# Kernel tuning notes

Measured on AMD Instinct MI355X. Metric: run time of the kernel, lower is better.

Reference implementation:

```python
import jax, jax.numpy as jnp
import numpy as np

T = 8
TAU = 2.0       # spikingjelly LIFNode default tau
VTH = 1.0       # default v_threshold
ALPHA = 2.0     # surrogate.ATan alpha
EPS = 1e-5      # BatchNorm eps


@jax.custom_vjp
def spike_fn(x):
    # Heaviside with ATan surrogate gradient
    return (x >= 0.0).astype(x.dtype)

def _spike_fwd(x):
    return (x >= 0.0).astype(x.dtype), x

def _spike_bwd(x, g):
    sg = (ALPHA / 2.0) / (1.0 + (jnp.pi / 2.0 * ALPHA * x) ** 2)
    return (g * sg,)

spike_fn.defvjp(_spike_fwd, _spike_bwd)


def lif(x_seq):
    """Multi-step LIF over leading time axis. decay_input=True, hard reset to 0, detach_reset."""
    def step(v, x):
        v = v + (x - v) / TAU            # charge
        s = spike_fn(v - VTH)            # fire (surrogate grad)
        v = v * (1.0 - jax.lax.stop_gradient(s))  # detached hard reset to v_reset=0
        return v, s
    _, s_seq = jax.lax.scan(step, jnp.zeros_like(x_seq[0]), x_seq)
    return s_seq


def conv2d(x, w, b, stride):
    y = jax.lax.conv_general_dilated(x, w, (stride, stride), 'VALID',
                                     dimension_numbers=('NCHW', 'OIHW', 'NCHW'))
    return y + b[None, :, None, None]


def batchnorm(x, g, b):
    # training-mode BN over merged (T*B, H, W) axes, matching step_mode='m' BatchNorm2d
    m = x.mean((0, 2, 3), keepdims=True)
    v = x.var((0, 2, 3), keepdims=True)
    return g[None, :, None, None] * (x - m) * jax.lax.rsqrt(v + EPS) + b[None, :, None, None]


def setup_inputs() -> dict:
    key = jax.random.key(0)
    ks = jax.random.split(key, 12)
    def w_init(k, shape):
        fan_in = int(np.prod(shape[1:]))
        return jax.random.normal(k, shape, dtype=jnp.float32) / np.sqrt(fan_in)
    x = jax.random.normal(ks[0], (128, 4, 84, 84), dtype=jnp.float32)
    return {
        'x': x,
        'conv1_w': w_init(ks[1], (32, 4, 8, 8)),  'conv1_b': jnp.zeros((32,), jnp.float32),
        'bn1_g': jnp.ones((32,), jnp.float32),    'bn1_b': jnp.zeros((32,), jnp.float32),
        'conv2_w': w_init(ks[2], (64, 32, 4, 4)), 'conv2_b': jnp.zeros((64,), jnp.float32),
        'bn2_g': jnp.ones((64,), jnp.float32),    'bn2_b': jnp.zeros((64,), jnp.float32),
        'conv3_w': w_init(ks[3], (64, 64, 3, 3)), 'conv3_b': jnp.zeros((64,), jnp.float32),
        'bn3_g': jnp.ones((64,), jnp.float32),    'bn3_b': jnp.zeros((64,), jnp.float32),
        'fc1_w': w_init(ks[4], (512, 3136)),      'fc1_b': jnp.zeros((512,), jnp.float32),
        'fco_w': w_init(ks[5], (2, 512)),         'fco_b': jnp.zeros((2,), jnp.float32),
    }


def reference(x, conv1_w, conv1_b, bn1_g, bn1_b, conv2_w, conv2_b, bn2_g, bn2_b,
              conv3_w, conv3_b, bn3_g, bn3_b, fc1_w, fc1_b, fco_w, fco_b):
    B = x.shape[0]
    # replicate input over T timesteps; fold T into batch for conv/BN (step_mode='m')
    xs = jnp.broadcast_to(x, (T,) + x.shape).reshape((T * B,) + x.shape[1:])

    h = batchnorm(conv2d(xs, conv1_w, conv1_b, 4), bn1_g, bn1_b)   # [TB,32,20,20]
    s = lif(h.reshape((T, B) + h.shape[1:]))
    h = s.reshape((T * B,) + s.shape[2:])

    h = batchnorm(conv2d(h, conv2_w, conv2_b, 2), bn2_g, bn2_b)    # [TB,64,9,9]
    s = lif(h.reshape((T, B) + h.shape[1:]))
    h = s.reshape((T * B,) + s.shape[2:])

    h = batchnorm(conv2d(h, conv3_w, conv3_b, 1), bn3_g, bn3_b)    # [TB,64,7,7]
    s = lif(h.reshape((T, B) + h.shape[1:]))                        # [T,B,64,7,7]

    feat = s.reshape(T, B, -1)                                      # [T,B,3136]
    hid = lif(jnp.einsum('tbi,oi->tbo', feat, fc1_w) + fc1_b)       # [T,B,512]
    out_seq = jnp.einsum('tbo,ko->tbk', hid, fco_w) + fco_b         # [T,B,2]
    return out_seq.mean(0)                                          # [B,2]
```

## Files before the change

kernel.cpp:

```cpp
#include <hip/hip_runtime.h>
#include <cstdint>
#include <cstddef>

#define TT 8

#define E2_ELEMS (128*64*81)
#define E3_ELEMS (128*64*49)

typedef __attribute__((ext_vector_type(8))) short short8;
typedef __attribute__((ext_vector_type(4))) short short4v;
typedef __attribute__((ext_vector_type(4))) float f32x4;

#define BAR_LDS() do { asm volatile("s_waitcnt lgkmcnt(0)" ::: "memory"); \
                       __builtin_amdgcn_s_barrier(); } while (0)

__device__ __forceinline__ void gld_lds16(const void* g, void* l) {
  __builtin_amdgcn_global_load_lds((const __attribute__((address_space(1))) void*)g,
                                   (__attribute__((address_space(3))) void*)l, 16, 0, 0);
}

__device__ __forceinline__ void split3(float v, ushort& h, ushort& m, ushort& l) {
  union { __bf16 b; ushort u; } H, M, L;
  H.b = (__bf16)v; float r1 = v - (float)H.b;
  M.b = (__bf16)r1; float r2 = r1 - (float)M.b;
  L.b = (__bf16)r2;
  h = H.u; m = M.u; l = L.u;
}

__device__ __forceinline__ short8 ld8(const ushort* p) {
  union { short4v h[2]; short8 v; } U;
  U.h[0] = *(const short4v*)(p);
  U.h[1] = *(const short4v*)(p + 4);
  return U.v;
}

__device__ __forceinline__ void bn_wave_stats(const float* __restrict__ p0,
                                              const float* __restrict__ p1,
                                              int ln, float n,
                                              float* __restrict__ stm,
                                              float* __restrict__ str, int cl) {
  float a0 = p0[ln]       + p0[ln + 256];
  float a2 = p0[ln + 128] + p0[ln + 384];
  float a1 = p0[ln + 64]  + p0[ln + 320];
  float a3 = p0[ln + 192] + p0[ln + 448];
  float s  = (a0 + a2) + (a1 + a3);
  float q0 = p1[ln]       + p1[ln + 256];
  float q2 = p1[ln + 128] + p1[ln + 384];
  float q1 = p1[ln + 64]  + p1[ln + 320];
  float q3 = p1[ln + 192] + p1[ln + 448];
  float sq = (q0 + q2) + (q1 + q3);
  #pragma unroll
  for (int mask = 32; mask >= 1; mask >>= 1) {
    s  += __shfl_xor(s,  mask);
    sq += __shfl_xor(sq, mask);
  }
  if (ln == 0) {
    float m = s / n;
    float var = sq / n - m * m;
    stm[cl] = m;
    str[cl] = rsqrtf(var + 1e-5f);
  }
}

__global__ __launch_bounds__(256) void prep_all(const float* __restrict__ w1,
                                                const float* __restrict__ w2,
                                                const float* __restrict__ w3,
                                                const float* __restrict__ wfc,
                                                __bf16* __restrict__ w1f,
                                                __bf16* __restrict__ w2f,
                                                __bf16* __restrict__ w3f,
                                                __bf16* __restrict__ wff) {
  __shared__ float tile[12544];
  int bxx = blockIdx.x;
  int tid = threadIdx.x;

  if (bxx >= 912) {
    int bx2 = bxx - 912;
    int oc0 = (bx2 >> 3) * 32;
    int ci0 = (bx2 & 7) * 8;
    for (int f = tid; f < 12544; f += 256) {
      int oc_l = f / 392, r = f - oc_l * 392;
      tile[f] = wfc[(size_t)(oc0 + oc_l) * 3136 + ci0 * 49 + r];
    }
    __syncthreads();
    int squad = (ci0 & 31) >> 3;
    int sadd  = ci0 >> 5;
    for (int g = tid; g < 1568; g += 256) {
      int pos = g >> 5, oc_l = g & 31;
      union { __bf16 h[8]; uint4 u; } T0, T1, T2;
      #pragma unroll
      for (int j = 0; j < 8; j++) {
        float wv = tile[oc_l * 392 + j * 49 + pos];
        float hf = (float)(__bf16)wv;
        float r1 = wv - hf;
        float mf = (float)(__bf16)r1;
        float r2 = r1 - mf;
        T0.h[j] = (__bf16)wv; T1.h[j] = (__bf16)r1; T2.h[j] = (__bf16)r2;
      }
      int s = pos * 2 + sadd;
      size_t b0 = (((size_t)s * 4 + squad) * 512 + oc0 + oc_l) * 8;
      *(uint4*)(wff + b0)           = T0.u;
      *(uint4*)(wff + b0 + 1605632) = T1.u;
      *(uint4*)(wff + b0 + 3211264) = T2.u;
    }
    return;
  }

  int i = bxx * 256 + tid;
  if (i < 98304) {
    int v = i;
    int j    = v & 7;
    int oc   = (v >> 3) & 63;
    int quad = (v >> 9) & 3;
    int ksg  = (v >> 11) & 15;
    int term = v >> 15;
    int k = ksg * 32 + quad * 8 + j;
    int ci = k >> 4, kpos = k & 15;
    float w = w2[oc * 512 + ci * 16 + kpos];
    float hf = (float)(__bf16)w;
    float r1 = w - hf;
    float mf = (float)(__bf16)r1;
    float r2 = r1 - mf;
    w2f[v] = (term == 0) ? (__bf16)w : (term == 1) ? (__bf16)r1 : (__bf16)r2;
  } else if (i < 208896) {
    int v = i - 98304;
    int j    = v & 7;
    int oc   = (v >> 3) & 63;
    int quad = (v >> 9) & 3;
    int tk   = v >> 11;
    int term = tk / 18, kstep = tk % 18;
    int k = kstep * 32 + quad * 8 + j;
    int pos = k >> 6, ci = k & 63;
    float w = w3[oc * 576 + ci * 9 + pos];
    float hf = (float)(__bf16)w;
    float r1 = w - hf;
    float mf = (float)(__bf16)r1;
    float r2 = r1 - mf;
    w3f[v] = (term == 0) ? (__bf16)w : (term == 1) ? (__bf16)r1 : (__bf16)r2;
  } else {
    int v = i - 208896;
    int j    = v & 7;
    int oc   = (v >> 3) & 31;
    int quad = (v >> 8) & 3;
    int ks   = (v >> 10) & 7;
    int term = v >> 13;
    int k = ks * 32 + quad * 8 + j;
    float w = w1[oc * 256 + k];
    float hf = (float)(__bf16)w;
    float r1 = w - hf;
    float mf = (float)(__bf16)r1;
    float r2 = r1 - mf;
    w1f[v] = (term == 0) ? (__bf16)w : (term == 1) ? (__bf16)r1 : (__bf16)r2;
  }
}

__global__ __launch_bounds__(128) void k_conv1m(const float* __restrict__ x,
                                                const __bf16* __restrict__ w1f,
                                                const float* __restrict__ bias,
                                                float* __restrict__ out,
                                                float* __restrict__ pout) {
  __shared__ ushort xs[24192];
  int tid = threadIdx.x;
  int bx = blockIdx.x;
  int img = bx >> 2, q = bx & 3;
  const float* xb = x + (size_t)img * 28224 + q * 1680;
  for (int f = tid; f < 2016; f += 128) {
    int ci = f / 504, rr = f - ci * 504;
    int row = rr / 21, c4 = rr - row * 21;
    float4 v4 = *(const float4*)(xb + ci * 7056 + row * 84 + c4 * 4);
    union { ushort s[4]; uint2 u; } H, M, L;
    float vv[4] = {v4.x, v4.y, v4.z, v4.w};
    #pragma unroll
    for (int j = 0; j < 4; j++) split3(vv[j], H.s[j], M.s[j], L.s[j]);
    int eo = ci * 2016 + row * 84 + c4 * 4;
    *(uint2*)(xs + eo)         = H.u;
    *(uint2*)(xs + 8064 + eo)  = M.u;
    *(uint2*)(xs + 16128 + eo) = L.u;
  }
  __syncthreads();
  int nh = tid >> 6, lane = tid & 63;
  int l15 = lane & 15, quad = lane >> 4;
  int aoff[7];
  #pragma unroll
  for (int mt = 0; mt < 7; mt++) {
    int px = mt * 16 + l15; if (px > 99) px = 99;
    int oy = px / 20, ox = px - oy * 20;
    aoff[mt] = oy * 336 + ox * 4;
  }
  f32x4 acc[7];
  #pragma unroll
  for (int mt = 0; mt < 7; mt++) acc[mt] = (f32x4){0.f, 0.f, 0.f, 0.f};
  const __bf16* wpb = w1f + quad * 256 + (nh * 16 + l15) * 8;
  for (int ks = 0; ks < 8; ks++) {
    const __bf16* wp = wpb + ks * 1024;
    short8 bh = *(const short8*)(wp);
    short8 bm = *(const short8*)(wp + 8192);
    short8 bl = *(const short8*)(wp + 16384);
    int pair = ks * 4 + quad;
    int e0 = (pair >> 3) * 2016 + (pair & 7) * 84;
    short8 ah[7], am[7], al[7];
    #pragma unroll
    for (int mt = 0; mt < 7; mt++) {
      int e = e0 + aoff[mt];
      ah[mt] = ld8(xs + e);
      am[mt] = ld8(xs + 8064 + e);
      al[mt] = ld8(xs + 16128 + e);
    }
    #pragma unroll
    for (int mt = 0; mt < 7; mt++)
      acc[mt] = __builtin_amdgcn_mfma_f32_16x16x32_bf16(ah[mt], bh, acc[mt], 0, 0, 0);
    #pragma unroll
    for (int mt = 0; mt < 7; mt++)
      acc[mt] = __builtin_amdgcn_mfma_f32_16x16x32_bf16(ah[mt], bm, acc[mt], 0, 0, 0);
    #pragma unroll
    for (int mt = 0; mt < 7; mt++)
      acc[mt] = __builtin_amdgcn_mfma_f32_16x16x32_bf16(am[mt], bh, acc[mt], 0, 0, 0);
    #pragma unroll
    for (int mt = 0; mt < 7; mt++)
      acc[mt] = __builtin_amdgcn_mfma_f32_16x16x32_bf16(am[mt], bm, acc[mt], 0, 0, 0);
    #pragma unroll
    for (int mt = 0; mt < 7; mt++)
      acc[mt] = __builtin_amdgcn_mfma_f32_16x16x32_bf16(ah[mt], bl, acc[mt], 0, 0, 0);
    #pragma unroll
    for (int mt = 0; mt < 7; mt++)
      acc[mt] = __builtin_amdgcn_mfma_f32_16x16x32_bf16(al[mt], bh, acc[mt], 0, 0, 0);
    #pragma unroll
    for (int mt = 0; mt < 7; mt++)
      acc[mt] = __builtin_amdgcn_mfma_f32_16x16x32_bf16(am[mt], bl, acc[mt], 0, 0, 0);
    #pragma unroll
    for (int mt = 0; mt < 7; mt++)
      acc[mt] = __builtin_amdgcn_mfma_f32_16x16x32_bf16(al[mt], bm, acc[mt], 0, 0, 0);
  }
  int oc = nh * 16 + l15;
  float bv = bias[oc];
  float sl = 0.f, sl2 = 0.f;
  float* op = out + (size_t)img * 12800 + oc * 400 + q * 100;
  #pragma unroll
  for (int mt = 0; mt < 7; mt++) {
    int pxb = mt * 16 + quad * 4;
    #pragma unroll
    for (int r = 0; r < 4; r++) {
      int px = pxb + r;
      if (px < 100) {
        float v = acc[mt][r] + bv;
        op[px] = v;
        sl += v; sl2 += v * v;
      }
    }
  }
  __syncthreads();
  float* sred = (float*)xs;
  sred[oc * 4 + quad] = sl;
  sred[128 + oc * 4 + quad] = sl2;
  __syncthreads();
  if (tid < 32) {
    float s  = sred[tid*4] + sred[tid*4+1] + sred[tid*4+2] + sred[tid*4+3];
    float s2 = sred[128+tid*4] + sred[128+tid*4+1] + sred[128+tid*4+2] + sred[128+tid*4+3];
    pout[tid * 512 + bx] = s;
    pout[16384 + tid * 512 + bx] = s2;
  }
}

__global__ void k_bnfinal2(const float* __restrict__ pin, int sqoff, float n,
                           float* __restrict__ meanArr, float* __restrict__ rstdArr) {
  __shared__ float l0[256], l1[256];
  int c = blockIdx.x, tid = threadIdx.x;
  l0[tid] = pin[c * 512 + tid] + pin[c * 512 + tid + 256];
  l1[tid] = pin[sqoff + c * 512 + tid] + pin[sqoff + c * 512 + tid + 256];
  __syncthreads();
  for (int k = 128; k > 0; k >>= 1) {
    if (tid < k) { l0[tid] += l0[tid + k]; l1[tid] += l1[tid + k]; }
    __syncthreads();
  }
  if (tid == 0) {
    float m = l0[0] / n;
    float var = l1[0] / n - m * m;
    meanArr[c] = m;
    rstdArr[c] = rsqrtf(var + 1e-5f);
  }
}

__global__ void k_lif1b(const float* __restrict__ h, const float* __restrict__ mean,
                        const float* __restrict__ rstd, const float* __restrict__ g,
                        const float* __restrict__ bb, uint32_t* __restrict__ sout) {
  int idx = blockIdx.x * 256 + threadIdx.x;
  int ic = idx / 20;
  int ci = ic & 31;
  const float* hp = h + (size_t)idx * 20;
  float gm = g[ci], mm = mean[ci], rs = rstd[ci], bc = bb[ci];
  float xv[20];
  #pragma unroll
  for (int j4 = 0; j4 < 5; j4++) {
    float4 hv = ((const float4*)hp)[j4];
    xv[j4 * 4 + 0] = gm * (hv.x - mm) * rs + bc;
    xv[j4 * 4 + 1] = gm * (hv.y - mm) * rs + bc;
    xv[j4 * 4 + 2] = gm * (hv.z - mm) * rs + bc;
    xv[j4 * 4 + 3] = gm * (hv.w - mm) * rs + bc;
  }
  float v[20];
  #pragma unroll
  for (int j = 0; j < 20; j++) v[j] = 0.f;
  #pragma unroll
  for (int t = 0; t < TT; t++) {
    uint32_t w = 0;
    #pragma unroll
    for (int j = 0; j < 20; j++) {
      v[j] = v[j] + (xv[j] - v[j]) * 0.5f;
      uint32_t s = (v[j] >= 1.0f);
      w |= s << j;
      if (s) v[j] = 0.f;
    }
    sout[t * 81920 + idx] = w;
  }
}

__global__ __launch_bounds__(256) void k_conv2m(const uint32_t* __restrict__ s1b,
                                                const __bf16* __restrict__ wf,
                                                const float* __restrict__ bias,
                                                float* __restrict__ out,
                                                float* __restrict__ pout) {
  __shared__ uint32_t sp[1280];
  __shared__ uint4 wl4[3072];
  __bf16* wl = (__bf16*)wl4;
  int tid = threadIdx.x;
  int img0 = blockIdx.x * 2;
  {
    const uint32_t* src = s1b + (size_t)img0 * 640;
    for (int i = tid; i < 1280; i += 256) sp[i] = src[i];
  }
  int wave = tid >> 6, lane = tid & 63;
  int img_local = wave >> 1;
  int nh = wave & 1;
  int l15 = lane & 15, quad = lane >> 4;
  int ci_off = quad >> 1;
  int kyp = (quad & 1) * 2;
  int spb[6], sh[6];
  #pragma unroll
  for (int mt = 0; mt < 6; mt++) {
    int px = mt * 16 + l15;
    if (px > 80) px = 80;
    int oy = px / 9, ox = px - oy * 9;
    sh[mt]  = ox * 2;
    spb[mt] = img_local * 640 + ci_off * 20 + oy * 2 + kyp;
  }
  f32x4 acc[6][2];
  #pragma unroll
  for (int mt = 0; mt < 6; mt++)
    #pragma unroll
    for (int nt = 0; nt < 2; nt++) acc[mt][nt] = (f32x4){0.f, 0.f, 0.f, 0.f};

  for (int kc = 0; kc < 4; kc++) {
    __syncthreads();
    for (int o = tid * 8; o < 24576; o += 2048) {
      int tk = o >> 11;
      int term = tk >> 2, ksl = tk & 3;
      const __bf16* src = wf + (((term * 16 + kc * 4 + ksl)) << 11) + (o & 2047);
      gld_lds16(src, wl + o);
    }
    __syncthreads();
    #pragma unroll
    for (int ks = 0; ks < 4; ks++) {
      int ksg = kc * 4 + ks;
      short8 a[6];
      #pragma unroll
      for (int mt = 0; mt < 6; mt++) {
        uint32_t w0 = sp[spb[mt] + ksg * 40];
        uint32_t w1 = sp[spb[mt] + ksg * 40 + 1];
        uint32_t n0 = (w0 >> sh[mt]) & 15u;
        uint32_t n1 = (w1 >> sh[mt]) & 15u;
        union { uint32_t u[4]; short8 v; } A;
        A.u[0] = ((n0 & 1u) ? 0x3F80u : 0u) | ((n0 & 2u) ? 0x3F800000u : 0u);
        A.u[1] = ((n0 & 4u) ? 0x3F80u : 0u) | ((n0 & 8u) ? 0x3F800000u : 0u);
        A.u[2] = ((n1 & 1u) ? 0x3F80u : 0u) | ((n1 & 2u) ? 0x3F800000u : 0u);
        A.u[3] = ((n1 & 4u) ? 0x3F80u : 0u) | ((n1 & 8u) ? 0x3F800000u : 0u);
        a[mt] = A.v;
      }
      #pragma unroll
      for (int term = 0; term < 3; term++) {
        int fb = ((term * 4 + ks) << 11) + (quad << 9);
        #pragma unroll
        for (int nt = 0; nt < 2; nt++) {
          short8 b = *(const short8*)(wl + fb + ((((nh << 1) | nt) << 4) + l15) * 8);
          #pragma unroll
          for (int mt = 0; mt < 6; mt++)
            acc[mt][nt] = __builtin_amdgcn_mfma_f32_16x16x32_bf16(a[mt], b, acc[mt][nt], 0, 0, 0);
        }
      }
    }
  }
  float sl[2], sl2[2];
  #pragma unroll
  for (int nt = 0; nt < 2; nt++) {
    sl[nt] = 0.f; sl2[nt] = 0.f;
    int oc = nh * 32 + nt * 16 + l15;
    float bv = bias[oc];
    float* op = out + ((size_t)(img0 + img_local) * 64 + oc) * 81;
    #pragma unroll
    for (int mt = 0; mt < 6; mt++) {
      int pxr = mt * 16 + quad * 4;
      #pragma unroll
      for (int r = 0; r < 4; r++) {
        int px = pxr + r;
        if (px < 81) {
          float v = acc[mt][nt][r] + bv;
          op[px] = v;
          sl[nt] += v; sl2[nt] += v * v;
        }
      }
    }
  }
  __syncthreads();
  float* sred = (float*)wl4;
  #pragma unroll
  for (int nt = 0; nt < 2; nt++) {
    int oc = nh * 32 + nt * 16 + l15;
    int idx = oc * 8 + img_local * 4 + quad;
    sred[idx] = sl[nt];
    sred[512 + idx] = sl2[nt];
  }
  __syncthreads();
  if (tid < 64) {
    float s = 0.f, s2 = 0.f;
    #pragma unroll
    for (int k = 0; k < 8; k++) { s += sred[tid * 8 + k]; s2 += sred[512 + tid * 8 + k]; }
    pout[tid * 512 + blockIdx.x] = s;
    pout[32768 + tid * 512 + blockIdx.x] = s2;
  }
}

__global__ __launch_bounds__(256) void k_lifb2T(const float* __restrict__ h,
                                                const float* __restrict__ bnp,
                                                const float* __restrict__ g,
                                                const float* __restrict__ bb,
                                                uint32_t* __restrict__ s2T) {
  __shared__ uint32_t sb[288];
  __shared__ float stm[32], str[32];
  int b = blockIdx.x, half = blockIdx.y;
  int tid = threadIdx.x;
  int wavei = tid >> 6, ln = tid & 63;
  for (int cl = wavei; cl < 32; cl += 4) {
    int c = half * 32 + cl;
    bn_wave_stats(bnp + c * 512, bnp + 32768 + c * 512, ln, 82944.f, stm, str, cl);
  }
  __syncthreads();
  int c1 = half * 32 + tid / 9, py1 = tid % 9;
  bool has2 = tid < 32;
  int r2 = tid + 256;
  int c2i = half * 32 + r2 / 9, py2 = r2 % 9;
  float gm1 = g[c1], mm1 = stm[tid / 9], rs1 = str[tid / 9], bc1 = bb[c1];
  float gm2 = 0.f, mm2 = 0.f, rs2 = 0.f, bc2 = 0.f;
  if (has2) { gm2 = g[c2i]; mm2 = stm[r2 / 9]; rs2 = str[r2 / 9]; bc2 = bb[c2i]; }
  float v1[9], v2[9];
  #pragma unroll
  for (int j = 0; j < 9; j++) { v1[j] = 0.f; v2[j] = 0.f; }
  size_t base1 = ((size_t)b * 64 + c1) * 81 + py1 * 9;
  size_t base2 = has2 ? ((size_t)b * 64 + c2i) * 81 + py2 * 9 : base1;
  float c1v[9], c2v[9];
  {
    const float* hp = h;
    #pragma unroll
    for (int j = 0; j < 9; j++) c1v[j] = hp[base1 + j];
    if (has2) {
      #pragma unroll
      for (int j = 0; j < 9; j++) c2v[j] = hp[base2 + j];
    }
  }
  #pragma unroll 1
  for (int t = 0; t < TT; t++) {
    float n1v[9], n2v[9];
    if (t < TT - 1) {
      const float* hp = h + (size_t)(t + 1) * E2_ELEMS;
      #pragma unroll
      for (int j = 0; j < 9; j++) n1v[j] = hp[base1 + j];
      if (has2) {
        #pragma unroll
        for (int j = 0; j < 9; j++) n2v[j] = hp[base2 + j];
      }
    }
    uint32_t w = 0;
    #pragma unroll
    for (int j = 0; j < 9; j++) {
      float xv = gm1 * (c1v[j] - mm1) * rs1 + bc1;
      v1[j] = v1[j] + (xv - v1[j]) * 0.5f;
      uint32_t s = (v1[j] >= 1.0f);
      w |= s << j;
      if (s) v1[j] = 0.f;
    }
    sb[tid] = w;
    if (has2) {
      uint32_t w2 = 0;
      #pragma unroll
      for (int j = 0; j < 9; j++) {
        float xv = gm2 * (c2v[j] - mm2) * rs2 + bc2;
        v2[j] = v2[j] + (xv - v2[j]) * 0.5f;
        uint32_t s = (v2[j] >= 1.0f);
        w2 |= s << j;
        if (s) v2[j] = 0.f;
      }
      sb[r2] = w2;
    }
    BAR_LDS();
    if (tid < 81) {
      int r = tid / 9, cpix = tid - r * 9;
      uint32_t wo = 0;
      #pragma unroll
      for (int ci = 0; ci < 32; ci++)
        wo |= ((sb[ci * 9 + r] >> cpix) & 1u) << ci;
      s2T[(size_t)(t * 128 + b) * 162 + tid * 2 + half] = wo;
    }
    BAR_LDS();
    if (t < TT - 1) {
      #pragma unroll
      for (int j = 0; j < 9; j++) c1v[j] = n1v[j];
      if (has2) {
        #pragma unroll
        for (int j = 0; j < 9; j++) c2v[j] = n2v[j];
      }
    }
  }
}

__global__ __launch_bounds__(256) void k_conv3m(const uint32_t* __restrict__ s2T,
                                                const __bf16* __restrict__ wf,
                                                const float* __restrict__ bias,
                                                float* __restrict__ out,
                                                float* __restrict__ pout) {
  __shared__ uint32_t sp[324];
  __shared__ uint4 wl4[4608];
  __bf16* wl = (__bf16*)wl4;
  int tid = threadIdx.x;
  int img0 = blockIdx.x * 2;
  {
    const uint32_t* src = s2T + (size_t)img0 * 162;
    for (int i = tid; i < 324; i += 256) sp[i] = src[i];
  }
  int wave = tid >> 6, lane = tid & 63;
  int img_local = wave >> 1, nh = wave & 1;
  int l15 = lane & 15, quad = lane >> 4;
  int qsh = quad * 8;
  int base[4];
  #pragma unroll
  for (int mt = 0; mt < 4; mt++) {
    int px = mt * 16 + l15;
    if (px > 48) px = 48;
    int oy = px / 7, ox = px - oy * 7;
    base[mt] = img_local * 162 + (oy * 9 + ox) * 2;
  }
  f32x4 acc[4][2];
  #pragma unroll
  for (int mt = 0; mt < 4; mt++)
    #pragma unroll
    for (int nt = 0; nt < 2; nt++) acc[mt][nt] = (f32x4){0.f, 0.f, 0.f, 0.f};

  #pragma unroll
  for (int kc = 0; kc < 3; kc++) {
    __syncthreads();
    #pragma unroll
    for (int it = 0; it < 18; it++) {
      const __bf16* s = wf + (((it / 6) * 18 + kc * 6 + (it % 6)) << 11) + tid * 8;
      gld_lds16(s, wl + (it << 11) + tid * 8);
    }
    __syncthreads();
    #pragma unroll
    for (int ksl = 0; ksl < 6; ksl++) {
      int kstep = kc * 6 + ksl;
      int pos = kstep >> 1, cihalf = kstep & 1;
      int ky = pos / 3, kx = pos % 3;
      short8 a[4];
      #pragma unroll
      for (int mt = 0; mt < 4; mt++) {
        uint32_t word = sp[base[mt] + (ky * 9 + kx) * 2 + cihalf];
        uint32_t byt = (word >> qsh) & 255u;
        union { uint32_t u[4]; short8 v; } A;
        A.u[0] = ((byt & 1u)  ? 0x3F80u : 0u) | ((byt & 2u)   ? 0x3F800000u : 0u);
        A.u[1] = ((byt & 4u)  ? 0x3F80u : 0u) | ((byt & 8u)   ? 0x3F800000u : 0u);
        A.u[2] = ((byt & 16u) ? 0x3F80u : 0u) | ((byt & 32u)  ? 0x3F800000u : 0u);
        A.u[3] = ((byt & 64u) ? 0x3F80u : 0u) | ((byt & 128u) ? 0x3F800000u : 0u);
        a[mt] = A.v;
      }
      #pragma unroll
      for (int term = 0; term < 3; term++) {
        int fb = ((term * 6 + ksl) << 11) + (quad << 9);
        #pragma unroll
        for (int nt = 0; nt < 2; nt++) {
          short8 b = *(const short8*)(wl + fb + ((((nh << 1) | nt) << 4) + l15) * 8);
          #pragma unroll
          for (int mt = 0; mt < 4; mt++)
            acc[mt][nt] = __builtin_amdgcn_mfma_f32_16x16x32_bf16(a[mt], b, acc[mt][nt], 0, 0, 0);
        }
      }
    }
  }
  float sl[2], sl2[2];
  #pragma unroll
  for (int nt = 0; nt < 2; nt++) {
    sl[nt] = 0.f; sl2[nt] = 0.f;
    int oc = nh * 32 + nt * 16 + l15;
    float bv = bias[oc];
    float* op = out + ((size_t)(img0 + img_local) * 64 + oc) * 49;
    #pragma unroll
    for (int mt = 0; mt < 4; mt++) {
      int pxr = mt * 16 + quad * 4;
      #pragma unroll
      for (int r = 0; r < 4; r++) {
        int px = pxr + r;
        if (px < 49) {
          float v = acc[mt][nt][r] + bv;
          op[px] = v;
          sl[nt] += v; sl2[nt] += v * v;
        }
      }
    }
  }
  __syncthreads();
  float* sred = (float*)wl4;
  #pragma unroll
  for (int nt = 0; nt < 2; nt++) {
    int oc = nh * 32 + nt * 16 + l15;
    int idx = oc * 8 + img_local * 4 + quad;
    sred[idx] = sl[nt];
    sred[512 + idx] = sl2[nt];
  }
  __syncthreads();
  if (tid < 64) {
    float s = 0.f, s2 = 0.f;
    #pragma unroll
    for (int k = 0; k < 8; k++) { s += sred[tid * 8 + k]; s2 += sred[512 + tid * 8 + k]; }
    pout[tid * 512 + blockIdx.x] = s;
    pout[32768 + tid * 512 + blockIdx.x] = s2;
  }
}

__global__ __launch_bounds__(256) void k_lifb3T(const float* __restrict__ h,
                                                const float* __restrict__ bnp,
                                                const float* __restrict__ g,
                                                const float* __restrict__ bb,
                                                uint32_t* __restrict__ s3T) {
  __shared__ uint32_t sb[224];
  __shared__ float stm[32], str[32];
  int b = blockIdx.x, half = blockIdx.y;
  int tid = threadIdx.x;
  int wavei = tid >> 6, ln = tid & 63;
  for (int cl = wavei; cl < 32; cl += 4) {
    int c = half * 32 + cl;
    bn_wave_stats(bnp + c * 512, bnp + 32768 + c * 512, ln, 50176.f, stm, str, cl);
  }
  __syncthreads();
  bool active = tid < 224;
  int row = active ? tid : 0;
  int c = half * 32 + row / 7, py = row % 7;
  float gm = g[c], mm = stm[row / 7], rs = str[row / 7], bc = bb[c];
  float v[7];
  #pragma unroll
  for (int j = 0; j < 7; j++) v[j] = 0.f;
  size_t base = ((size_t)b * 64 + c) * 49 + py * 7;
  float cv[7];
  if (active) {
    #pragma unroll
    for (int j = 0; j < 7; j++) cv[j] = h[base + j];
  }
  #pragma unroll 1
  for (int t = 0; t < TT; t++) {
    float nv[7];
    if (active && t < TT - 1) {
      const float* hp = h + (size_t)(t + 1) * E3_ELEMS;
      #pragma unroll
      for (int j = 0; j < 7; j++) nv[j] = hp[base + j];
    }
    if (active) {
      uint32_t w = 0;
      #pragma unroll
      for (int j = 0; j < 7; j++) {
        float xv = gm * (cv[j] - mm) * rs + bc;
        v[j] = v[j] + (xv - v[j]) * 0.5f;
        uint32_t s = (v[j] >= 1.0f);
        w |= s << j;
        if (s) v[j] = 0.f;
      }
      sb[tid] = w;
    }
    BAR_LDS();
    if (tid < 49) {
      int py2 = tid / 7, px = tid - py2 * 7;
      uint32_t wo = 0;
      #pragma unroll
      for (int ci = 0; ci < 32; ci++)
        wo |= ((sb[ci * 7 + py2] >> px) & 1u) << ci;
      s3T[(size_t)(t * 128 + b) * 98 + tid * 2 + half] = wo;
    }
    BAR_LDS();
    if (active && t < TT - 1) {
      #pragma unroll
      for (int j = 0; j < 7; j++) cv[j] = nv[j];
    }
  }
}

__global__ __launch_bounds__(256) void k_fc1m(const uint32_t* __restrict__ s3T,
                                              const __bf16* __restrict__ wf,
                                              float* __restrict__ f1) {
  __shared__ uint32_t aS[6272];
  int tid = threadIdx.x;
  int row0 = blockIdx.x * 64;
  int oc0  = blockIdx.y * 16;
  {
    const uint32_t* src = s3T + (size_t)row0 * 98;
    for (int i = tid; i < 6272; i += 256) aS[i] = src[i];
  }
  __syncthreads();
  int wave = tid >> 6, lane = tid & 63;
  int l15 = lane & 15, quad = lane >> 4;
  int qsh = quad * 8;
  f32x4 acc[4];
  #pragma unroll
  for (int mt = 0; mt < 4; mt++) acc[mt] = (f32x4){0.f, 0.f, 0.f, 0.f};
  int nIter = (wave < 2) ? 25 : 24;
  #pragma unroll 2
  for (int i = 0; i < nIter; i++) {
    int ks = i * 4 + wave;
    short8 a[4];
    #pragma unroll
    for (int mt = 0; mt < 4; mt++) {
      uint32_t word = aS[(mt * 16 + l15) * 98 + ks];
      uint32_t byt = (word >> qsh) & 255u;
      union { uint32_t u[4]; short8 v; } A;
      A.u[0] = ((byt & 1u)  ? 0x3F80u : 0u) | ((byt & 2u)   ? 0x3F800000u : 0u);
      A.u[1] = ((byt & 4u)  ? 0x3F80u : 0u) | ((byt & 8u)   ? 0x3F800000u : 0u);
      A.u[2] = ((byt & 16u) ? 0x3F80u : 0u) | ((byt & 32u)  ? 0x3F800000u : 0u);
      A.u[3] = ((byt & 64u) ? 0x3F80u : 0u) | ((byt & 128u) ? 0x3F800000u : 0u);
      a[mt] = A.v;
    }
    #pragma unroll
    for (int term = 0; term < 3; term++) {
      size_t fb = ((size_t)((term * 98 + ks) * 4 + quad) * 512 + oc0 + l15) * 8;
      short8 b = *(const short8*)(wf + fb);
      #pragma unroll
      for (int mt = 0; mt < 4; mt++)
        acc[mt] = __builtin_amdgcn_mfma_f32_16x16x32_bf16(a[mt], b, acc[mt], 0, 0, 0);
    }
  }
  __syncthreads();
  float* red = (float*)aS;
  #pragma unroll
  for (int mt = 0; mt < 4; mt++)
    #pragma unroll
    for (int r = 0; r < 4; r++)
      red[(wave * 64 + lane) * 17 + mt * 4 + r] = acc[mt][r];
  __syncthreads();
  #pragma unroll
  for (int k = 0; k < 4; k++) {
    int oi = tid + k * 256;
    int row_l = oi >> 4, oc_l = oi & 15;
    int mt = row_l >> 4, rem = row_l & 15;
    int q2 = rem >> 2, r = rem & 3;
    int ln = q2 * 16 + oc_l;
    float s = red[(0 * 64 + ln) * 17 + mt * 4 + r];
    s += red[(1 * 64 + ln) * 17 + mt * 4 + r];
    s += red[(2 * 64 + ln) * 17 + mt * 4 + r];
    s += red[(3 * 64 + ln) * 17 + mt * 4 + r];
    f1[(size_t)(row0 + row_l) * 512 + oc0 + oc_l] = s;
  }
}

__global__ __launch_bounds__(256) void k_fc1fco(const float* __restrict__ f1,
                                                const float* __restrict__ bias,
                                                const float* __restrict__ w,
                                                const float* __restrict__ fcob,
                                                float* __restrict__ out) {
  int b = blockIdx.x, tid = threadIdx.x;
  int o0 = tid, o1 = tid + 256;
  float bv0 = bias[o0], bv1 = bias[o1];
  float w00 = w[o0], w10 = w[512 + o0];
  float w01 = w[o1], w11 = w[512 + o1];
  float x0[TT], x1[TT];
  #pragma unroll
  for (int t = 0; t < TT; t++) {
    x0[t] = f1[(size_t)(t * 128 + b) * 512 + o0];
    x1[t] = f1[(size_t)(t * 128 + b) * 512 + o1];
  }
  float v0 = 0.f, v1 = 0.f;
  float a0 = 0.f, a1 = 0.f;
  #pragma unroll
  for (int t = 0; t < TT; t++) {
    float s0 = x0[t] + bv0;
    v0 = v0 + (s0 - v0) * 0.5f;
    bool sp0 = (v0 >= 1.0f);
    if (sp0) v0 = 0.f;
    float s1 = x1[t] + bv1;
    v1 = v1 + (s1 - v1) * 0.5f;
    bool sp1 = (v1 >= 1.0f);
    if (sp1) v1 = 0.f;
    if (sp0) { a0 += w00; a1 += w10; }
    if (sp1) { a0 += w01; a1 += w11; }
  }
  __shared__ float l0[256], l1[256];
  l0[tid] = a0; l1[tid] = a1; __syncthreads();
  for (int k = 128; k > 0; k >>= 1) {
    if (tid < k) { l0[tid] += l0[tid + k]; l1[tid] += l1[tid + k]; }
    __syncthreads();
  }
  if (tid == 0) {
    out[b * 2 + 0] = l0[0] * 0.125f + fcob[0];
    out[b * 2 + 1] = l1[0] * 0.125f + fcob[1];
  }
}

extern "C" void kernel_launch(void* const* d_in, const int* in_sizes, int n_in,
                              void* d_out, int out_size, void* d_ws, size_t ws_size,
                              hipStream_t stream) {
  const float* x    = (const float*)d_in[0];
  const float* c1w  = (const float*)d_in[1];
  const float* c1b  = (const float*)d_in[2];
  const float* bn1g = (const float*)d_in[3];
  const float* bn1b = (const float*)d_in[4];
  const float* c2w  = (const float*)d_in[5];
  const float* c2b  = (const float*)d_in[6];
  const float* bn2g = (const float*)d_in[7];
  const float* bn2b = (const float*)d_in[8];
  const float* c3w  = (const float*)d_in[9];
  const float* c3b  = (const float*)d_in[10];
  const float* bn3g = (const float*)d_in[11];
  const float* bn3b = (const float*)d_in[12];
  const float* fc1w = (const float*)d_in[13];
  const float* fc1b = (const float*)d_in[14];
  const float* fcow = (const float*)d_in[15];
  const float* fcob = (const float*)d_in[16];
  float* out = (float*)d_out;

  char* ws = (char*)d_ws;
  float*    h1     = (float*)(ws + 0);
  uint32_t* s1bits = (uint32_t*)(ws + 6553600);
  float*    h2     = (float*)(ws + 19660800);
  float*    h3     = (float*)(ws + 46202880);
  __bf16*   w2f    = (__bf16*)(ws + 60882944);
  __bf16*   w3f    = (__bf16*)(ws + 61079552);
  uint32_t* s2T    = (uint32_t*)(ws + 61300736);
  __bf16*   w1f    = (__bf16*)(ws + 62390272);
  float*    st     = (float*)(ws + 64880640);
  __bf16*   wff    = (__bf16*)(ws + 67108864);
  float*    f1sum  = (float*)(ws + 76742656);
  uint32_t* s3T    = (uint32_t*)(ws + 85131264);
  float*    bnpA   = (float*)(ws + 85532672);
  float*    bnpB   = (float*)(ws + 85794816);

  prep_all   <<<1040, 256, 0, stream>>>(c1w, c2w, c3w, fc1w, w1f, w2f, w3f, wff);

  k_conv1m   <<<512, 128, 0, stream>>>(x, w1f, c1b, h1, bnpA);
  k_bnfinal2 <<<32, 256, 0, stream>>>(bnpA, 16384, 51200.f, st, st + 32);
  k_lif1b    <<<320, 256, 0, stream>>>(h1, st, st + 32, bn1g, bn1b, s1bits);

  k_conv2m   <<<512, 256, 0, stream>>>(s1bits, w2f, c2b, h2, bnpB);
  k_lifb2T   <<<dim3(128, 2), 256, 0, stream>>>(h2, bnpB, bn2g, bn2b, s2T);

  k_conv3m   <<<512, 256, 0, stream>>>(s2T, w3f, c3b, h3, bnpB);
  k_lifb3T   <<<dim3(128, 2), 256, 0, stream>>>(h3, bnpB, bn3g, bn3b, s3T);

  k_fc1m     <<<dim3(16, 32), 256, 0, stream>>>(s3T, wff, f1sum);
  k_fc1fco   <<<128, 256, 0, stream>>>(f1sum, fc1b, fcow, fcob, out);
}
```

Baseline: 238.4 us.

## Double-buffer conv2/conv3 weight staging to overlap loads with MFMA

Replaces the large chunked weight staging in the conv2 and conv3 kernels with per-k-step double buffering. The next k-step's weights are fetched into one LDS buffer while MFMAs run on the other, with a vmcnt+barrier between steps. This is meant to hide global-to-LDS load latency and shrink LDS use from 48-72KB to 24KB per block, which may raise occupancy. The cost is more barriers, one per k-step instead of one per chunk.

Result: slower. 243.3 us (+2.1%).

```diff
diff --git a/kernel.cpp b/kernel.cpp
--- a/kernel.cpp
+++ b/kernel.cpp
@@ -13,6 +13,9 @@
 
 #define BAR_LDS() do { asm volatile("s_waitcnt lgkmcnt(0)" ::: "memory"); \
                        __builtin_amdgcn_s_barrier(); } while (0)
+
+#define BAR_VM() do { asm volatile("s_waitcnt vmcnt(0) lgkmcnt(0)" ::: "memory"); \
+                      __builtin_amdgcn_s_barrier(); } while (0)
 
 __device__ __forceinline__ void gld_lds16(const void* g, void* l) {
   __builtin_amdgcn_global_load_lds((const __attribute__((address_space(1))) void*)g,
@@ -320,8 +323,10 @@
                                                 float* __restrict__ out,
                                                 float* __restrict__ pout) {
   __shared__ uint32_t sp[1280];
-  __shared__ uint4 wl4[3072];
-  __bf16* wl = (__bf16*)wl4;
+  __shared__ uint4 bufA4[768];
+  __shared__ uint4 bufB4[768];
+  __bf16* bufA = (__bf16*)bufA4;
+  __bf16* bufB = (__bf16*)bufB4;
   int tid = threadIdx.x;
   int img0 = blockIdx.x * 2;
   {
@@ -349,45 +354,53 @@
     #pragma unroll
     for (int nt = 0; nt < 2; nt++) acc[mt][nt] = (f32x4){0.f, 0.f, 0.f, 0.f};
 
-  for (int kc = 0; kc < 4; kc++) {
-    __syncthreads();
-    for (int o = tid * 8; o < 24576; o += 2048) {
-      int tk = o >> 11;
-      int term = tk >> 2, ksl = tk & 3;
-      const __bf16* src = wf + (((term * 16 + kc * 4 + ksl)) << 11) + (o & 2047);
-      gld_lds16(src, wl + o);
-    }
-    __syncthreads();
-    #pragma unroll
-    for (int ks = 0; ks < 4; ks++) {
-      int ksg = kc * 4 + ks;
-      short8 a[6];
-      #pragma unroll
-      for (int mt = 0; mt < 6; mt++) {
-        uint32_t w0 = sp[spb[mt] + ksg * 40];
-        uint32_t w1 = sp[spb[mt] + ksg * 40 + 1];
-        uint32_t n0 = (w0 >> sh[mt]) & 15u;
-        uint32_t n1 = (w1 >> sh[mt]) & 15u;
-        union { uint32_t u[4]; short8 v; } A;
-        A.u[0] = ((n0 & 1u) ? 0x3F80u : 0u) | ((n0 & 2u) ? 0x3F800000u : 0u);
-        A.u[1] = ((n0 & 4u) ? 0x3F80u : 0u) | ((n0 & 8u) ? 0x3F800000u : 0u);
-        A.u[2] = ((n1 & 1u) ? 0x3F80u : 0u) | ((n1 & 2u) ? 0x3F800000u : 0u);
-        A.u[3] = ((n1 & 4u) ? 0x3F80u : 0u) | ((n1 & 8u) ? 0x3F800000u : 0u);
-        a[mt] = A.v;
-      }
-      #pragma unroll
-      for (int term = 0; term < 3; term++) {
-        int fb = ((term * 4 + ks) << 11) + (quad << 9);
+  auto STAGE = [&](int ksg, __bf16* dst) {
+    #pragma unroll
+    for (int term = 0; term < 3; term++)
+      gld_lds16(wf + (((term * 16 + ksg)) << 11) + tid * 8, dst + term * 2048 + tid * 8);
+  };
+  auto COMPUTE = [&](int ksg, const __bf16* wl) {
+    short8 a[6];
+    #pragma unroll
+    for (int mt = 0; mt < 6; mt++) {
+      uint32_t w0 = sp[spb[mt] + ksg * 40];
+      uint32_t w1 = sp[spb[mt] + ksg * 40 + 1];
+      uint32_t n0 = (w0 >> sh[mt]) & 15u;
+      uint32_t n1 = (w1 >> sh[mt]) & 15u;
+      union { uint32_t u[4]; short8 v; } A;
+      A.u[0] = ((n0 & 1u) ? 0x3F80u : 0u) | ((n0 & 2u) ? 0x3F800000u : 0u);
+      A.u[1] = ((n0 & 4u) ? 0x3F80u : 0u) | ((n0 & 8u) ? 0x3F800000u : 0u);
+      A.u[2] = ((n1 & 1u) ? 0x3F80u : 0u) | ((n1 & 2u) ? 0x3F800000u : 0u);
+      A.u[3] = ((n1 & 4u) ? 0x3F80u : 0u) | ((n1 & 8u) ? 0x3F800000u : 0u);
+      a[mt] = A.v;
+    }
+    #pragma unroll
+    for (int term = 0; term < 3; term++) {
+      int fb = (term << 11) + (quad << 9);
+      #pragma unroll
+      for (int nt = 0; nt < 2; nt++) {
+        short8 b = *(const short8*)(wl + fb + ((((nh << 1) | nt) << 4) + l15) * 8);
         #pragma unroll
-        for (int nt = 0; nt < 2; nt++) {
-          short8 b = *(const short8*)(wl + fb + ((((nh << 1) | nt) << 4) + l15) * 8);
-          #pragma unroll
-          for (int mt = 0; mt < 6; mt++)
-            acc[mt][nt] = __builtin_amdgcn_mfma_f32_16x16x32_bf16(a[mt], b, acc[mt][nt], 0, 0, 0);
-        }
-      }
-    }
-  }
+        for (int mt = 0; mt < 6; mt++)
+          acc[mt][nt] = __builtin_amdgcn_mfma_f32_16x16x32_bf16(a[mt], b, acc[mt][nt], 0, 0, 0);
+      }
+    }
+  };
+
+  STAGE(0, bufA);
+  __syncthreads();
+  #pragma unroll 1
+  for (int kp = 0; kp < 8; kp++) {
+    int ksgA = kp * 2;
+    STAGE(ksgA + 1, bufB);
+    COMPUTE(ksgA, bufA);
+    BAR_VM();
+    int ksgB = ksgA + 1;
+    if (ksgB < 15) STAGE(ksgB + 1, bufA);
+    COMPUTE(ksgB, bufB);
+    BAR_VM();
+  }
+
   float sl[2], sl2[2];
   #pragma unroll
   for (int nt = 0; nt < 2; nt++) {
@@ -410,7 +423,7 @@
     }
   }
   __syncthreads();
-  float* sred = (float*)wl4;
+  float* sred = (float*)bufA4;
   #pragma unroll
   for (int nt = 0; nt < 2; nt++) {
     int oc = nh * 32 + nt * 16 + l15;
@@ -526,8 +539,10 @@
                                                 float* __restrict__ out,
                                                 float* __restrict__ pout) {
   __shared__ uint32_t sp[324];
-  __shared__ uint4 wl4[4608];
-  __bf16* wl = (__bf16*)wl4;
+  __shared__ uint4 bufA4[768];
+  __shared__ uint4 bufB4[768];
+  __bf16* bufA = (__bf16*)bufA4;
+  __bf16* bufB = (__bf16*)bufB4;
   int tid = threadIdx.x;
   int img0 = blockIdx.x * 2;
   {
@@ -552,45 +567,53 @@
     #pragma unroll
     for (int nt = 0; nt < 2; nt++) acc[mt][nt] = (f32x4){0.f, 0.f, 0.f, 0.f};
 
-  #pragma unroll
-  for (int kc = 0; kc < 3; kc++) {
-    __syncthreads();
-    #pragma unroll
-    for (int it = 0; it < 18; it++) {
-      const __bf16* s = wf + (((it / 6) * 18 + kc * 6 + (it % 6)) << 11) + tid * 8;
-      gld_lds16(s, wl + (it << 11) + tid * 8);
-    }
-    __syncthreads();
-    #pragma unroll
-    for (int ksl = 0; ksl < 6; ksl++) {
-      int kstep = kc * 6 + ksl;
-      int pos = kstep >> 1, cihalf = kstep & 1;
-      int ky = pos / 3, kx = pos % 3;
-      short8 a[4];
-      #pragma unroll
-      for (int mt = 0; mt < 4; mt++) {
-        uint32_t word = sp[base[mt] + (ky * 9 + kx) * 2 + cihalf];
-        uint32_t byt = (word >> qsh) & 255u;
-        union { uint32_t u[4]; short8 v; } A;
-        A.u[0] = ((byt & 1u)  ? 0x3F80u : 0u) | ((byt & 2u)   ? 0x3F800000u : 0u);
-        A.u[1] = ((byt & 4u)  ? 0x3F80u : 0u) | ((byt & 8u)   ? 0x3F800000u : 0u);
-        A.u[2] = ((byt & 16u) ? 0x3F80u : 0u) | ((byt & 32u)  ? 0x3F800000u : 0u);
-        A.u[3] = ((byt & 64u) ? 0x3F80u : 0u) | ((byt & 128u) ? 0x3F800000u : 0u);
-        a[mt] = A.v;
-      }
-      #pragma unroll
-      for (int term = 0; term < 3; term++) {
-        int fb = ((term * 6 + ksl) << 11) + (quad << 9);
+  auto STAGE3 = [&](int kstep, __bf16* dst) {
+    #pragma unroll
+    for (int term = 0; term < 3; term++)
+      gld_lds16(wf + (((term * 18 + kstep)) << 11) + tid * 8, dst + term * 2048 + tid * 8);
+  };
+  auto COMPUTE3 = [&](int kstep, const __bf16* wl) {
+    int pos = kstep >> 1, cihalf = kstep & 1;
+    int ky = pos / 3, kx = pos % 3;
+    short8 a[4];
+    #pragma unroll
+    for (int mt = 0; mt < 4; mt++) {
+      uint32_t word = sp[base[mt] + (ky * 9 + kx) * 2 + cihalf];
+      uint32_t byt = (word >> qsh) & 255u;
+      union { uint32_t u[4]; short8 v; } A;
+      A.u[0] = ((byt & 1u)  ? 0x3F80u : 0u) | ((byt & 2u)   ? 0x3F800000u : 0u);
+      A.u[1] = ((byt & 4u)  ? 0x3F80u : 0u) | ((byt & 8u)   ? 0x3F800000u : 0u);
+      A.u[2] = ((byt & 16u) ? 0x3F80u : 0u) | ((byt & 32u)  ? 0x3F800000u : 0u);
+      A.u[3] = ((byt & 64u) ? 0x3F80u : 0u) | ((byt & 128u) ? 0x3F800000u : 0u);
+      a[mt] = A.v;
+    }
+    #pragma unroll
+    for (int term = 0; term < 3; term++) {
+      int fb = (term << 11) + (quad << 9);
+      #pragma unroll
+      for (int nt = 0; nt < 2; nt++) {
+        short8 b = *(const short8*)(wl + fb + ((((nh << 1) | nt) << 4) + l15) * 8);
         #pragma unroll
-        for (int nt = 0; nt < 2; nt++) {
-          short8 b = *(const short8*)(wl + fb + ((((nh << 1) | nt) << 4) + l15) * 8);
-          #pragma unroll
-          for (int mt = 0; mt < 4; mt++)
-            acc[mt][nt] = __builtin_amdgcn_mfma_f32_16x16x32_bf16(a[mt], b, acc[mt][nt], 0, 0, 0);
-        }
-      }
-    }
-  }
+        for (int mt = 0; mt < 4; mt++)
+          acc[mt][nt] = __builtin_amdgcn_mfma_f32_16x16x32_bf16(a[mt], b, acc[mt][nt], 0, 0, 0);
+      }
+    }
+  };
+
+  STAGE3(0, bufA);
+  __syncthreads();
+  #pragma unroll 1
+  for (int kp = 0; kp < 9; kp++) {
+    int kA = kp * 2;
+    STAGE3(kA + 1, bufB);
+    COMPUTE3(kA, bufA);
+    BAR_VM();
+    int kB = kA + 1;
+    if (kB < 17) STAGE3(kB + 1, bufA);
+    COMPUTE3(kB, bufB);
+    BAR_VM();
+  }
+
   float sl[2], sl2[2];
   #pragma unroll
   for (int nt = 0; nt < 2; nt++) {
@@ -613,7 +636,7 @@
     }
   }
   __syncthreads();
-  float* sred = (float*)wl4;
+  float* sred = (float*)bufA4;
   #pragma unroll
   for (int nt = 0; nt < 2; nt++) {
     int oc = nh * 32 + nt * 16 + l15;
```

## Split conv2/conv3 M tiles across twice as many waves per block

Applied to the files above, without the earlier changes.

Doubles the conv2 and conv3 blocks from 256 to 512 threads. Each wave pair now splits the pixel (M) tiles in half, so each wave holds fewer accumulators and more waves are resident to hide latency. The weight staging load is spread across the larger block. The per-channel BN partial sums now go through an LDS exchange between the two half-waves before the existing reduction, which adds an extra barrier and LDS traffic. Each B fragment read from LDS is also reused by fewer MFMAs.

After: 239.9 us. About the same (+0.6%).

```diff
diff --git a/kernel.cpp b/kernel.cpp
--- a/kernel.cpp
+++ b/kernel.cpp
@@ -314,11 +314,11 @@
   }
 }
 
-__global__ __launch_bounds__(256) void k_conv2m(const uint32_t* __restrict__ s1b,
-                                                const __bf16* __restrict__ wf,
-                                                const float* __restrict__ bias,
-                                                float* __restrict__ out,
-                                                float* __restrict__ pout) {
+__global__ __launch_bounds__(512, 4) void k_conv2m(const uint32_t* __restrict__ s1b,
+                                                   const __bf16* __restrict__ wf,
+                                                   const float* __restrict__ bias,
+                                                   float* __restrict__ out,
+                                                   float* __restrict__ pout) {
   __shared__ uint32_t sp[1280];
   __shared__ uint4 wl4[3072];
   __bf16* wl = (__bf16*)wl4;
@@ -326,32 +326,33 @@
   int img0 = blockIdx.x * 2;
   {
     const uint32_t* src = s1b + (size_t)img0 * 640;
-    for (int i = tid; i < 1280; i += 256) sp[i] = src[i];
+    for (int i = tid; i < 1280; i += 512) sp[i] = src[i];
   }
   int wave = tid >> 6, lane = tid & 63;
-  int img_local = wave >> 1;
-  int nh = wave & 1;
+  int img_local = wave >> 2;
+  int nh = (wave >> 1) & 1;
+  int mh = wave & 1;
   int l15 = lane & 15, quad = lane >> 4;
   int ci_off = quad >> 1;
   int kyp = (quad & 1) * 2;
-  int spb[6], sh[6];
-  #pragma unroll
-  for (int mt = 0; mt < 6; mt++) {
-    int px = mt * 16 + l15;
+  int spb[3], sh[3];
+  #pragma unroll
+  for (int mt = 0; mt < 3; mt++) {
+    int px = (mh * 3 + mt) * 16 + l15;
     if (px > 80) px = 80;
     int oy = px / 9, ox = px - oy * 9;
     sh[mt]  = ox * 2;
     spb[mt] = img_local * 640 + ci_off * 20 + oy * 2 + kyp;
   }
-  f32x4 acc[6][2];
-  #pragma unroll
-  for (int mt = 0; mt < 6; mt++)
+  f32x4 acc[3][2];
+  #pragma unroll
+  for (int mt = 0; mt < 3; mt++)
     #pragma unroll
     for (int nt = 0; nt < 2; nt++) acc[mt][nt] = (f32x4){0.f, 0.f, 0.f, 0.f};
 
   for (int kc = 0; kc < 4; kc++) {
     __syncthreads();
-    for (int o = tid * 8; o < 24576; o += 2048) {
+    for (int o = tid * 8; o < 24576; o += 4096) {
       int tk = o >> 11;
       int term = tk >> 2, ksl = tk & 3;
       const __bf16* src = wf + (((term * 16 + kc * 4 + ksl)) << 11) + (o & 2047);
@@ -361,9 +362,9 @@
     #pragma unroll
     for (int ks = 0; ks < 4; ks++) {
       int ksg = kc * 4 + ks;
-      short8 a[6];
-      #pragma unroll
-      for (int mt = 0; mt < 6; mt++) {
+      short8 a[3];
+      #pragma unroll
+      for (int mt = 0; mt < 3; mt++) {
         uint32_t w0 = sp[spb[mt] + ksg * 40];
         uint32_t w1 = sp[spb[mt] + ksg * 40 + 1];
         uint32_t n0 = (w0 >> sh[mt]) & 15u;
@@ -382,41 +383,65 @@
         for (int nt = 0; nt < 2; nt++) {
           short8 b = *(const short8*)(wl + fb + ((((nh << 1) | nt) << 4) + l15) * 8);
           #pragma unroll
-          for (int mt = 0; mt < 6; mt++)
+          for (int mt = 0; mt < 3; mt++)
             acc[mt][nt] = __builtin_amdgcn_mfma_f32_16x16x32_bf16(a[mt], b, acc[mt][nt], 0, 0, 0);
         }
       }
     }
   }
-  float sl[2], sl2[2];
+  __syncthreads();
+  float* vbuf = (float*)wl4;
+  float* sred = (float*)wl4 + 6144;
+  int g = ((img_local * 2 + nh) * 4 + quad) * 16 + l15;
+  float vloc[2][12];
   #pragma unroll
   for (int nt = 0; nt < 2; nt++) {
-    sl[nt] = 0.f; sl2[nt] = 0.f;
     int oc = nh * 32 + nt * 16 + l15;
     float bv = bias[oc];
     float* op = out + ((size_t)(img0 + img_local) * 64 + oc) * 81;
     #pragma unroll
-    for (int mt = 0; mt < 6; mt++) {
-      int pxr = mt * 16 + quad * 4;
+    for (int mtl = 0; mtl < 3; mtl++) {
       #pragma unroll
       for (int r = 0; r < 4; r++) {
-        int px = pxr + r;
-        if (px < 81) {
-          float v = acc[mt][nt][r] + bv;
-          op[px] = v;
-          sl[nt] += v; sl2[nt] += v * v;
+        int px = (mh * 3 + mtl) * 16 + quad * 4 + r;
+        float v = acc[mtl][nt][r] + bv;
+        if (px < 81) op[px] = v;
+        vloc[nt][mtl * 4 + r] = v;
+      }
+    }
+  }
+  if (mh == 1) {
+    #pragma unroll
+    for (int nt = 0; nt < 2; nt++)
+      #pragma unroll
+      for (int k = 0; k < 12; k++) vbuf[g * 24 + nt * 12 + k] = vloc[nt][k];
+  }
+  __syncthreads();
+  if (mh == 0) {
+    float sl[2], sl2[2];
+    #pragma unroll
+    for (int nt = 0; nt < 2; nt++) {
+      sl[nt] = 0.f; sl2[nt] = 0.f;
+      #pragma unroll
+      for (int mt = 0; mt < 6; mt++) {
+        #pragma unroll
+        for (int r = 0; r < 4; r++) {
+          int px = mt * 16 + quad * 4 + r;
+          if (px < 81) {
+            float v = (mt < 3) ? vloc[nt][mt * 4 + r]
+                               : vbuf[g * 24 + nt * 12 + (mt - 3) * 4 + r];
+            sl[nt] += v; sl2[nt] += v * v;
+          }
         }
       }
     }
-  }
-  __syncthreads();
-  float* sred = (float*)wl4;
-  #pragma unroll
-  for (int nt = 0; nt < 2; nt++) {
-    int oc = nh * 32 + nt * 16 + l15;
-    int idx = oc * 8 + img_local * 4 + quad;
-    sred[idx] = sl[nt];
-    sred[512 + idx] = sl2[nt];
+    #pragma unroll
+    for (int nt = 0; nt < 2; nt++) {
+      int oc = nh * 32 + nt * 16 + l15;
+      int idx = oc * 8 + img_local * 4 + quad;
+      sred[idx] = sl[nt];
+      sred[512 + idx] = sl2[nt];
+    }
   }
   __syncthreads();
   if (tid < 64) {
@@ -520,11 +545,11 @@
   }
 }
 
-__global__ __launch_bounds__(256) void k_conv3m(const uint32_t* __restrict__ s2T,
-                                                const __bf16* __restrict__ wf,
-                                                const float* __restrict__ bias,
-                                                float* __restrict__ out,
-                                                float* __restrict__ pout) {
+__global__ __launch_bounds__(512, 4) void k_conv3m(const uint32_t* __restrict__ s2T,
+                                                   const __bf16* __restrict__ wf,
+                                                   const float* __restrict__ bias,
+                                                   float* __restrict__ out,
+                                                   float* __restrict__ pout) {
   __shared__ uint32_t sp[324];
   __shared__ uint4 wl4[4608];
   __bf16* wl = (__bf16*)wl4;
@@ -532,23 +557,25 @@
   int img0 = blockIdx.x * 2;
   {
     const uint32_t* src = s2T + (size_t)img0 * 162;
-    for (int i = tid; i < 324; i += 256) sp[i] = src[i];
+    for (int i = tid; i < 324; i += 512) sp[i] = src[i];
   }
   int wave = tid >> 6, lane = tid & 63;
-  int img_local = wave >> 1, nh = wave & 1;
+  int img_local = wave >> 2;
+  int nh = (wave >> 1) & 1;
+  int mh = wave & 1;
   int l15 = lane & 15, quad = lane >> 4;
   int qsh = quad * 8;
-  int base[4];
-  #pragma unroll
-  for (int mt = 0; mt < 4; mt++) {
-    int px = mt * 16 + l15;
+  int base[2];
+  #pragma unroll
+  for (int mt = 0; mt < 2; mt++) {
+    int px = (mh * 2 + mt) * 16 + l15;
     if (px > 48) px = 48;
     int oy = px / 7, ox = px - oy * 7;
     base[mt] = img_local * 162 + (oy * 9 + ox) * 2;
   }
-  f32x4 acc[4][2];
-  #pragma unroll
-  for (int mt = 0; mt < 4; mt++)
+  f32x4 acc[2][2];
+  #pragma unroll
+  for (int mt = 0; mt < 2; mt++)
     #pragma unroll
     for (int nt = 0; nt < 2; nt++) acc[mt][nt] = (f32x4){0.f, 0.f, 0.f, 0.f};
 
@@ -556,9 +583,11 @@
   for (int kc = 0; kc < 3; kc++) {
     __syncthreads();
     #pragma unroll
-    for (int it = 0; it < 18; it++) {
-      const __bf16* s = wf + (((it / 6) * 18 + kc * 6 + (it % 6)) << 11) + tid * 8;
-      gld_lds16(s, wl + (it << 11) + tid * 8);
+    for (int it2 = 0; it2 < 9; it2++) {
+      int it = it2 * 2 + (tid >> 8);
+      int term = it / 6, ksl = it % 6;
+      const __bf16* s = wf + (((term * 18 + kc * 6 + ksl)) << 11) + (tid & 255) * 8;
+      gld_lds16(s, wl + (it << 11) + (tid & 255) * 8);
     }
     __syncthreads();
     #pragma unroll
@@ -566,9 +595,9 @@
       int kstep = kc * 6 + ksl;
       int pos = kstep >> 1, cihalf = kstep & 1;
       int ky = pos / 3, kx = pos % 3;
-      short8 a[4];
-      #pragma unroll
-      for (int mt = 0; mt < 4; mt++) {
+      short8 a[2];
+      #pragma unroll
+      for (int mt = 0; mt < 2; mt++) {
         uint32_t word = sp[base[mt] + (ky * 9 + kx) * 2 + cihalf];
         uint32_t byt = (word >> qsh) & 255u;
         union { uint32_t u[4]; short8 v; } A;
@@ -585,41 +614,65 @@
         for (int nt = 0; nt < 2; nt++) {
           short8 b = *(const short8*)(wl + fb + ((((nh << 1) | nt) << 4) + l15) * 8);
           #pragma unroll
-          for (int mt = 0; mt < 4; mt++)
+          for (int mt = 0; mt < 2; mt++)
             acc[mt][nt] = __builtin_amdgcn_mfma_f32_16x16x32_bf16(a[mt], b, acc[mt][nt], 0, 0, 0);
         }
       }
     }
   }
-  float sl[2], sl2[2];
+  __syncthreads();
+  float* vbuf = (float*)wl4;
+  float* sred = (float*)wl4 + 4096;
+  int g = ((img_local * 2 + nh) * 4 + quad) * 16 + l15;
+  float vloc[2][8];
   #pragma unroll
   for (int nt = 0; nt < 2; nt++) {
-    sl[nt] = 0.f; sl2[nt] = 0.f;
     int oc = nh * 32 + nt * 16 + l15;
     float bv = bias[oc];
     float* op = out + ((size_t)(img0 + img_local) * 64 + oc) * 49;
     #pragma unroll
-    for (int mt = 0; mt < 4; mt++) {
-      int pxr = mt * 16 + quad * 4;
+    for (int mtl = 0; mtl < 2; mtl++) {
       #pragma unroll
       for (int r = 0; r < 4; r++) {
-        int px = pxr + r;
-        if (px < 49) {
-          float v = acc[mt][nt][r] + bv;
-          op[px] = v;
-          sl[nt] += v; sl2[nt] += v * v;
+        int px = (mh * 2 + mtl) * 16 + quad * 4 + r;
+        float v = acc[mtl][nt][r] + bv;
+        if (px < 49) op[px] = v;
+        vloc[nt][mtl * 4 + r] = v;
+      }
+    }
+  }
+  if (mh == 1) {
+    #pragma unroll
+    for (int nt = 0; nt < 2; nt++)
+      #pragma unroll
+      for (int k = 0; k < 8; k++) vbuf[g * 16 + nt * 8 + k] = vloc[nt][k];
+  }
+  __syncthreads();
+  if (mh == 0) {
+    float sl[2], sl2[2];
+    #pragma unroll
+    for (int nt = 0; nt < 2; nt++) {
+      sl[nt] = 0.f; sl2[nt] = 0.f;
+      #pragma unroll
+      for (int mt = 0; mt < 4; mt++) {
+        #pragma unroll
+        for (int r = 0; r < 4; r++) {
+          int px = mt * 16 + quad * 4 + r;
+          if (px < 49) {
+            float v = (mt < 2) ? vloc[nt][mt * 4 + r]
+                               : vbuf[g * 16 + nt * 8 + (mt - 2) * 4 + r];
+            sl[nt] += v; sl2[nt] += v * v;
+          }
         }
       }
     }
-  }
-  __syncthreads();
-  float* sred = (float*)wl4;
-  #pragma unroll
-  for (int nt = 0; nt < 2; nt++) {
-    int oc = nh * 32 + nt * 16 + l15;
-    int idx = oc * 8 + img_local * 4 + quad;
-    sred[idx] = sl[nt];
-    sred[512 + idx] = sl2[nt];
+    #pragma unroll
+    for (int nt = 0; nt < 2; nt++) {
+      int oc = nh * 32 + nt * 16 + l15;
+      int idx = oc * 8 + img_local * 4 + quad;
+      sred[idx] = sl[nt];
+      sred[512 + idx] = sl2[nt];
+    }
   }
   __syncthreads();
   if (tid < 64) {
@@ -849,10 +902,10 @@
   k_bnfinal2 <<<32, 256, 0, stream>>>(bnpA, 16384, 51200.f, st, st + 32);
   k_lif1b    <<<320, 256, 0, stream>>>(h1, st, st + 32, bn1g, bn1b, s1bits);
 
-  k_conv2m   <<<512, 256, 0, stream>>>(s1bits, w2f, c2b, h2, bnpB);
+  k_conv2m   <<<512, 512, 0, stream>>>(s1bits, w2f, c2b, h2, bnpB);
   k_lifb2T   <<<dim3(128, 2), 256, 0, stream>>>(h2, bnpB, bn2g, bn2b, s2T);
 
-  k_conv3m   <<<512, 256, 0, stream>>>(s2T, w3f, c3b, h3, bnpB);
+  k_conv3m   <<<512, 512, 0, stream>>>(s2T, w3f, c3b, h3, bnpB);
   k_lifb3T   <<<dim3(128, 2), 256, 0, stream>>>(h3, bnpB, bn3g, bn3b, s3T);
 
   k_fc1m     <<<dim3(16, 32), 256, 0, stream>>>(s3T, wff, f1sum);
```
